# Optimization experiments

Measured on AMD Instinct MI355X. Metric: run time of the kernel, lower is better.

Reference implementation:

```python
import jax, jax.numpy as jnp
import numpy as np

N, E, G = 30000, 120000, 1000   # nodes, edges, graphs
IN, H, ED = 32, 64, 8           # in_dim, hidden, edge_dim


def setup_inputs() -> dict:
    key = jax.random.key(0)
    ks = iter(jax.random.split(key, 64))
    rn = lambda shp, s=0.05: jax.random.normal(next(ks), shp, dtype=jnp.float32) * s
    d = {}
    d["x"] = jax.random.normal(next(ks), (N, IN), dtype=jnp.float32)
    d["edge_index"] = jax.random.randint(next(ks), (2, E), 0, N)
    d["edge_attr"] = jax.random.normal(next(ks), (E, ED), dtype=jnp.float32)
    d["batch"] = jnp.sort(jax.random.randint(next(ks), (N,), 0, G))
    # layer 0: edge_nn maps edge_attr -> [H*IN], conv IN -> H
    d["ew1_0"] = rn((ED, H * IN)); d["eb1_0"] = jnp.zeros((H * IN,), jnp.float32)
    d["ew2_0"] = rn((H * IN, H * IN)); d["eb2_0"] = jnp.zeros((H * IN,), jnp.float32)
    d["root_0"] = rn((IN, H)); d["cb_0"] = jnp.zeros((H,), jnp.float32)
    # layers 1,2: edge_nn maps edge_attr -> [H*H], conv H -> H
    for i in (1, 2):
        d[f"ew1_{i}"] = rn((ED, H * H)); d[f"eb1_{i}"] = jnp.zeros((H * H,), jnp.float32)
        d[f"ew2_{i}"] = rn((H * H, H * H)); d[f"eb2_{i}"] = jnp.zeros((H * H,), jnp.float32)
        d[f"root_{i}"] = rn((H, H)); d[f"cb_{i}"] = jnp.zeros((H,), jnp.float32)
    # readout MLP
    d["mw1"] = rn((H, H)); d["mb1"] = jnp.zeros((H,), jnp.float32)
    d["mw2"] = rn((H, 1)); d["mb2"] = jnp.zeros((1,), jnp.float32)
    return d


def _nnconv(x, src, dst, edge_attr, ew1, eb1, ew2, eb2, root, cb, din, dout):
    # edge MLP -> per-edge weight matrix [E, din, dout]
    w = (jax.nn.relu(edge_attr @ ew1 + eb1) @ ew2 + eb2).reshape(-1, din, dout)
    # gather source features, per-edge matvec, scatter-mean to dest
    msg = jnp.einsum('ei,eio->eo', x[src], w)            # [E, dout]
    n = x.shape[0]
    s = jax.ops.segment_sum(msg, dst, num_segments=n)
    deg = jax.ops.segment_sum(jnp.ones((msg.shape[0],), msg.dtype), dst, num_segments=n)
    agg = s / jnp.maximum(deg, 1.0)[:, None]
    return agg + x @ root + cb


def reference(x, edge_index, edge_attr, batch,
              ew1_0, eb1_0, ew2_0, eb2_0, root_0, cb_0,
              ew1_1, eb1_1, ew2_1, eb2_1, root_1, cb_1,
              ew1_2, eb1_2, ew2_2, eb2_2, root_2, cb_2,
              mw1, mb1, mw2, mb2):
    src, dst = edge_index[0], edge_index[1]
    h = jax.nn.relu(_nnconv(x, src, dst, edge_attr, ew1_0, eb1_0, ew2_0, eb2_0, root_0, cb_0, IN, H))
    h = jax.nn.relu(_nnconv(h, src, dst, edge_attr, ew1_1, eb1_1, ew2_1, eb2_1, root_1, cb_1, H, H))
    h = jax.nn.relu(_nnconv(h, src, dst, edge_attr, ew1_2, eb1_2, ew2_2, eb2_2, root_2, cb_2, H, H))
    # global mean pool over graphs
    gs = jax.ops.segment_sum(h, batch, num_segments=G)
    cnt = jax.ops.segment_sum(jnp.ones((h.shape[0],), h.dtype), batch, num_segments=G)
    g = gs / jnp.maximum(cnt, 1.0)[:, None]
    # readout MLP (dropout inactive in eval)
    return jax.nn.relu(g @ mw1 + mb1) @ mw2 + mb2    # [G, 1]
```

## Files before the change

### kernel.cpp

```cpp
#include <hip/hip_runtime.h>
#include <cstdint>

#define N_TOT 30000
#define E_TOT 120000
#define G_TOT 1000

typedef unsigned short u16;
typedef unsigned int u32;
typedef __attribute__((ext_vector_type(8))) short short8;
typedef __attribute__((ext_vector_type(4))) float f32x4;

#define AS1 __attribute__((address_space(1)))
#define AS3 __attribute__((address_space(3)))

static __device__ __forceinline__ void gload_lds16(const void* g, void* l) {
  __builtin_amdgcn_global_load_lds((AS1 void*)(uintptr_t)g,
                                   (AS3 void*)(uint32_t)(uintptr_t)l, 16, 0, 0);
}

static __device__ __forceinline__ u16 f2bf(float f) {
  uint32_t u = __float_as_uint(f);
  uint32_t r = (u + 0x7fffu + ((u >> 16) & 1u)) >> 16;
  return (u16)r;
}
static __device__ __forceinline__ float bf2f(u16 v) {
  return __uint_as_float((uint32_t)v << 16);
}

__global__ void prep_kernel(const int* __restrict__ ei, const int* __restrict__ batch,
                            float* __restrict__ deg, float* __restrict__ gcnt,
                            int* __restrict__ sd) {
  int t = blockIdx.x * 256 + threadIdx.x;
  if (t < E_TOT) {
    atomicAdd(&deg[ei[E_TOT + t]], 1.0f);
    atomicAdd(&sd[ei[t]], 1);
  }
  if (t < N_TOT) atomicAdd(&gcnt[batch[t]], 1.0f);
}

__global__ void scan_kernel(const int* __restrict__ sd, int* __restrict__ off) {
  __shared__ int buf[1024];
  __shared__ int carry;
  const int t = threadIdx.x;
  if (t == 0) carry = 0;
  __syncthreads();
  for (int base = 0; base < N_TOT; base += 1024) {
    int v = base + t;
    int x = (v < N_TOT) ? sd[v] : 0;
    buf[t] = x;
    __syncthreads();
    for (int o = 1; o < 1024; o <<= 1) {
      int y = (t >= o) ? buf[t - o] : 0;
      __syncthreads();
      buf[t] += y;
      __syncthreads();
    }
    if (v < N_TOT) off[v] = carry + buf[t] - x;
    __syncthreads();
    if (t == 0) carry += buf[1023];
    __syncthreads();
  }
  if (t == 0) off[N_TOT] = carry;
}

__global__ void scatter_kernel(const int* __restrict__ ei, const float* __restrict__ ea,
                               const int* __restrict__ off, int* __restrict__ cur,
                               int* __restrict__ src_s, int* __restrict__ dst_s,
                               float* __restrict__ ea_s) {
  int e = blockIdx.x * 256 + threadIdx.x;
  if (e >= E_TOT) return;
  int s = ei[e];
  int pos = off[s] + atomicAdd(&cur[s], 1);
  src_s[pos] = s;
  dst_s[pos] = ei[E_TOT + e];
#pragma unroll
  for (int j = 0; j < 8; ++j) ea_s[(size_t)pos * 8 + j] = ea[(size_t)e * 8 + j];
}

__global__ void cvt_wp(const float* __restrict__ ew2, u16* __restrict__ wp,
                       int K, int DINp) {
  int idx = blockIdx.x * 256 + threadIdx.x;
  int c = idx & 127, kbh = idx >> 7;
  int kb = kbh >> 1, oh = kbh & 1;
  int k = kb * 4 + (c >> 5), o = oh * 32 + (c & 31);
  const float* src = ew2 + (size_t)k * (DINp * 64) + o;
  u16* dst = wp + (size_t)idx * DINp;
  for (int i = 0; i < DINp; ++i) dst[i] = f2bf(src[(size_t)i * 64]);
}

__global__ void cvt_w1(const float* __restrict__ ew1, float* __restrict__ ew1t, int K) {
  int i = blockIdx.x * 256 + threadIdx.x;
  if (i >= K * 8) return;
  int k = i >> 3, j = i & 7;
  ew1t[i] = ew1[(size_t)j * K + k];
}

template <int DIN>
__global__ __launch_bounds__(512, 4) void fused_conv(
    const u16* __restrict__ Wp, const float* __restrict__ ew1t,
    const float* __restrict__ eb1, const float* __restrict__ eb2,
    const float* __restrict__ xin, const float* __restrict__ eas,
    const int* __restrict__ src_s, const int* __restrict__ dst_s,
    const int* __restrict__ node_off, float* __restrict__ agg, int K) {
  constexpr int KF = DIN / 32;
  constexpr int NB = DIN / 8;
  constexpr int L_XB = 0;
  constexpr int L_WP = 64 * DIN * 2;
  constexpr int L_MS = L_WP + 128 * DIN * 2;
  constexpr int L_HS = L_MS + 16384;
  constexpr int L_VL = L_HS + 4096;
  __shared__ char smem[L_VL + 2048];

  const int t = threadIdx.x;
  const int lane = t & 63, wave = t >> 6;
  const int u = lane & 15, q = lane >> 4;
  const int grp = blockIdx.x >> 1, oh = blockIdx.x & 1;
  const int v0 = grp * 64;
  const int e0 = node_off[v0];
  const int v1 = (v0 + 64 < N_TOT) ? v0 + 64 : N_TOT;
  int Eblk = node_off[v1] - e0;
  if (Eblk > 512) Eblk = 512;

  {
    int row = t >> 3, i0 = (t & 7) * (DIN / 8);
    u16* xb = (u16*)(smem + L_XB) + row * DIN + i0;
    int vg = v0 + row;
#pragma unroll
    for (int j = 0; j < DIN / 8; ++j)
      xb[j] = (vg < N_TOT) ? f2bf(xin[(size_t)vg * DIN + i0 + j]) : (u16)0;
  }
  f32x4 ea0 = (f32x4){0.f, 0.f, 0.f, 0.f}, ea1 = (f32x4){0.f, 0.f, 0.f, 0.f};
  {
    int vl = 0;
    if (t < Eblk) {
      const f32x4* s = (const f32x4*)(eas + (size_t)(e0 + t) * 8);
      ea0 = s[0];
      ea1 = s[1];
      vl = src_s[e0 + t] - v0;
    }
    ((int*)(smem + L_VL))[t] = vl;
  }
  __syncthreads();

  short8 bfr[4][KF];
#pragma unroll
  for (int vt = 0; vt < 4; ++vt)
#pragma unroll
    for (int kf = 0; kf < KF; ++kf)
      bfr[vt][kf] =
          *(const short8*)(smem + L_XB + ((vt * 16 + u) * DIN + (kf * 4 + q) * 8) * 2);

  const int oq = t & 1;
  int vofs[2], vswz[2], slotp[2];
#pragma unroll
  for (int p = 0; p < 2; ++p) {
    int s = (t >> 1) + p * 256;
    slotp[p] = s;
    int vl = ((int*)(smem + L_VL))[s];
    vofs[p] = L_MS + vl * 256;
    vswz[p] = vl & 7;
  }
  f32x4 msg[2][4];
#pragma unroll
  for (int p = 0; p < 2; ++p)
#pragma unroll
    for (int j = 0; j < 4; ++j) msg[p][j] = (f32x4){0.f, 0.f, 0.f, 0.f};

  const size_t slab = (size_t)128 * DIN;
  const int nsteps = K >> 2;
  for (int kb = 0; kb < nsteps; ++kb) {
    const u16* gsl = Wp + (size_t)(kb * 2 + oh) * slab;
#pragma unroll
    for (int j = 0; j < NB / 4; ++j) {
      int s = j * 512 + t;
      int c = s / NB, ib = s % NB;
      gload_lds16(gsl + (c * NB + (ib ^ (c & (NB - 1)))) * 8, smem + L_WP + s * 16);
    }
    {
      const int kk = kb * 4;
      ushort4 hv;
      u16* hp = (u16*)&hv;
#pragma unroll
      for (int kc = 0; kc < 4; ++kc) {
        int k = kk + kc;
        const float* wr = ew1t + (size_t)k * 8;
        float a = eb1[k];
        a += ea0.x * wr[0] + ea0.y * wr[1] + ea0.z * wr[2] + ea0.w * wr[3];
        a += ea1.x * wr[4] + ea1.y * wr[5] + ea1.z * wr[6] + ea1.w * wr[7];
        hp[kc] = f2bf(a > 0.f ? a : 0.f);
      }
      *(ushort4*)(smem + L_HS + t * 8) = hv;
    }
    __syncthreads();

    {
      f32x4 acc[4];
#pragma unroll
      for (int vt = 0; vt < 4; ++vt) acc[vt] = (f32x4){0.f, 0.f, 0.f, 0.f};
      const int crow = wave * 16 + u;
#pragma unroll
      for (int kf = 0; kf < KF; ++kf) {
        short8 afr = *(const short8*)(
            smem + L_WP + (crow * DIN + (((kf * 4 + q) ^ (crow & (NB - 1))) * 8)) * 2);
#pragma unroll
        for (int vt = 0; vt < 4; ++vt)
          acc[vt] = __builtin_amdgcn_mfma_f32_16x16x32_bf16(afr, bfr[vt][kf], acc[vt], 0, 0, 0);
      }
#pragma unroll
      for (int vt = 0; vt < 4; ++vt) {
        int v = vt * 16 + u;
        uint2 pk;
        pk.x = ((u32)f2bf(acc[vt].y) << 16) | f2bf(acc[vt].x);
        pk.y = ((u32)f2bf(acc[vt].w) << 16) | f2bf(acc[vt].z);
        int bbG = ((wave << 1) | (q >> 1)) ^ (v & 7);
        *(uint2*)(smem + L_MS + v * 256 + bbG * 16 + (q & 1) * 8) = pk;
      }
    }
    __syncthreads();

#pragma unroll
    for (int p = 0; p < 2; ++p) {
      if (wave * 32 + p * 256 < Eblk) {
        ushort4 h4 = *(const ushort4*)(smem + L_HS + slotp[p] * 8);
        const u16* hp = (const u16*)&h4;
#pragma unroll
        for (int kc = 0; kc < 4; ++kc) {
          float h = bf2f(hp[kc]);
#pragma unroll
          for (int s = 0; s < 2; ++s) {
            int bb = (kc * 4 + oq * 2 + s) ^ vswz[p];
            uint4 m8 = *(const uint4*)(smem + vofs[p] + bb * 16);
            f32x4 lo, hi;
            lo.x = __uint_as_float(m8.x << 16);
            lo.y = __uint_as_float(m8.x & 0xffff0000u);
            lo.z = __uint_as_float(m8.y << 16);
            lo.w = __uint_as_float(m8.y & 0xffff0000u);
            hi.x = __uint_as_float(m8.z << 16);
            hi.y = __uint_as_float(m8.z & 0xffff0000u);
            hi.z = __uint_as_float(m8.w << 16);
            hi.w = __uint_as_float(m8.w & 0xffff0000u);
            msg[p][s * 2 + 0] += h * lo;
            msg[p][s * 2 + 1] += h * hi;
          }
        }
      }
    }
    __syncthreads();
  }

  {
    int v = t >> 3, o4 = (t & 7) * 4;
    f32x4 acc = (f32x4){0.f, 0.f, 0.f, 0.f};
    const u16* xb = (const u16*)(smem + L_XB) + v * DIN;
    const float* ep = eb2 + oh * 32 + o4;
    for (int i = 0; i < DIN; ++i) {
      float xv = bf2f(xb[i]);
      f32x4 w4 = *(const f32x4*)(ep + (size_t)i * 64);
      acc += xv * w4;
    }
    *(f32x4*)(smem + L_MS + (v * 32 + o4) * 4) = acc;
  }
  __syncthreads();

#pragma unroll
  for (int p = 0; p < 2; ++p) {
    int slot = slotp[p];
    if (slot < Eblk) {
      int d = dst_s[e0 + slot];
      int vl = (vofs[p] - L_MS) >> 8;
      float* ap = agg + (size_t)d * 64 + oh * 32 + oq * 16;
      const float* bt = (const float*)(smem + L_MS) + vl * 32 + oq * 16;
#pragma unroll
      for (int j = 0; j < 4; ++j) {
        f32x4 m = msg[p][j];
        atomicAdd(ap + j * 4 + 0, m.x + bt[j * 4 + 0]);
        atomicAdd(ap + j * 4 + 1, m.y + bt[j * 4 + 1]);
        atomicAdd(ap + j * 4 + 2, m.z + bt[j * 4 + 2]);
        atomicAdd(ap + j * 4 + 3, m.w + bt[j * 4 + 3]);
      }
    }
  }
}

__global__ void node_update(const float* __restrict__ agg, const float* __restrict__ deg,
                            const float* __restrict__ xin, const float* __restrict__ root,
                            const float* __restrict__ cbv, float* __restrict__ xout,
                            int din) {
  __shared__ float rl[4096];
  const int t = threadIdx.x;
  for (int i = t; i < din * 64; i += 256) rl[i] = root[i];
  __syncthreads();
  const int o = t & 63;
  const int n = blockIdx.x * 4 + (t >> 6);
  if (n >= N_TOT) return;
  float acc = cbv[o];
  for (int i = 0; i < din; ++i) acc += xin[(size_t)n * din + i] * rl[i * 64 + o];
  float d = deg[n];
  d = d > 1.f ? d : 1.f;
  acc += agg[(size_t)n * 64 + o] / d;
  xout[(size_t)n * 64 + o] = acc > 0.f ? acc : 0.f;
}

__global__ void pool_kernel(const float* __restrict__ x3, const int* __restrict__ batch,
                            float* __restrict__ gsum) {
  int t = blockIdx.x * 256 + threadIdx.x;
  if (t >= N_TOT * 64) return;
  int n = t >> 6, o = t & 63;
  atomicAdd(&gsum[(size_t)batch[n] * 64 + o], x3[t]);
}

__global__ void readout_kernel(const float* __restrict__ gsum, const float* __restrict__ gcnt,
                               const float* __restrict__ mw1, const float* __restrict__ mb1,
                               const float* __restrict__ mw2, const float* __restrict__ mb2,
                               float* __restrict__ out) {
  __shared__ float gv[4][64];
  const int t = threadIdx.x;
  const int o = t & 63, loc = t >> 6;
  const int g = blockIdx.x * 4 + loc;
  float v = 0.f;
  if (g < G_TOT) {
    float c = gcnt[g];
    c = c > 1.f ? c : 1.f;
    v = gsum[(size_t)g * 64 + o] / c;
  }
  gv[loc][o] = v;
  __syncthreads();
  float acc = mb1[o];
  for (int i = 0; i < 64; ++i) acc += gv[loc][i] * mw1[i * 64 + o];
  acc = acc > 0.f ? acc : 0.f;
  float p = acc * mw2[o];
#pragma unroll
  for (int off = 32; off > 0; off >>= 1) p += __shfl_down(p, off, 64);
  if (o == 0 && g < G_TOT) out[g] = p + mb2[0];
}

extern "C" void kernel_launch(void* const* d_in, const int* in_sizes, int n_in,
                              void* d_out, int out_size, void* d_ws, size_t ws_size,
                              hipStream_t stream) {
  const float* x     = (const float*)d_in[0];
  const int*   ei    = (const int*)d_in[1];
  const float* ea    = (const float*)d_in[2];
  const int*   batch = (const int*)d_in[3];
  const float* ew1[3] = {(const float*)d_in[4],  (const float*)d_in[10], (const float*)d_in[16]};
  const float* eb1[3] = {(const float*)d_in[5],  (const float*)d_in[11], (const float*)d_in[17]};
  const float* ew2[3] = {(const float*)d_in[6],  (const float*)d_in[12], (const float*)d_in[18]};
  const float* eb2[3] = {(const float*)d_in[7],  (const float*)d_in[13], (const float*)d_in[19]};
  const float* root[3] = {(const float*)d_in[8],  (const float*)d_in[14], (const float*)d_in[20]};
  const float* cbv[3]  = {(const float*)d_in[9],  (const float*)d_in[15], (const float*)d_in[21]};
  const float* mw1 = (const float*)d_in[22];
  const float* mb1 = (const float*)d_in[23];
  const float* mw2 = (const float*)d_in[24];
  const float* mb2 = (const float*)d_in[25];
  float* out = (float*)d_out;

  char* p = (char*)d_ws;
  auto carve = [&p](size_t bytes) {
    char* r = p;
    p += (bytes + 255) & ~(size_t)255;
    return r;
  };
  u16*   wp   = (u16*)carve((size_t)4096 * 64 * 64 * 2);
  float* ew1t = (float*)carve((size_t)4096 * 8 * 4);
  float* x1   = (float*)carve((size_t)N_TOT * 64 * 4);
  float* x2   = (float*)carve((size_t)N_TOT * 64 * 4);
  float* x3   = (float*)carve((size_t)N_TOT * 64 * 4);
  float* agg  = (float*)carve((size_t)N_TOT * 64 * 4);
  float* deg  = (float*)carve((size_t)N_TOT * 4);
  float* gsum = (float*)carve((size_t)G_TOT * 64 * 4);
  float* gcnt = (float*)carve((size_t)G_TOT * 4);
  int*   sd   = (int*)carve((size_t)N_TOT * 4);
  int*   noff = (int*)carve((size_t)(N_TOT + 1) * 4);
  int*   cur  = (int*)carve((size_t)N_TOT * 4);
  int*   srcs = (int*)carve((size_t)E_TOT * 4);
  int*   dsts = (int*)carve((size_t)E_TOT * 4);
  float* eass = (float*)carve((size_t)E_TOT * 8 * 4);

  hipMemsetAsync(deg, 0, (size_t)N_TOT * 4, stream);
  hipMemsetAsync(gsum, 0, (size_t)G_TOT * 64 * 4, stream);
  hipMemsetAsync(gcnt, 0, (size_t)G_TOT * 4, stream);
  hipMemsetAsync(sd, 0, (size_t)N_TOT * 4, stream);
  hipMemsetAsync(cur, 0, (size_t)N_TOT * 4, stream);

  prep_kernel<<<(E_TOT + 255) / 256, 256, 0, stream>>>(ei, batch, deg, gcnt, sd);
  scan_kernel<<<1, 1024, 0, stream>>>(sd, noff);
  scatter_kernel<<<(E_TOT + 255) / 256, 256, 0, stream>>>(ei, ea, noff, cur, srcs, dsts, eass);

  const float* xin_l[3]  = {x, x1, x2};
  float*       xout_l[3] = {x1, x2, x3};
  const int Ks[3]   = {2048, 4096, 4096};
  const int dins[3] = {32, 64, 64};
  const int grid_fused = ((N_TOT + 63) / 64) * 2;

  for (int L = 0; L < 3; ++L) {
    const int K = Ks[L], din = dins[L];
    cvt_wp<<<(K * 64) / 256, 256, 0, stream>>>(ew2[L], wp, K, din);
    cvt_w1<<<(K * 8 + 255) / 256, 256, 0, stream>>>(ew1[L], ew1t, K);
    hipMemsetAsync(agg, 0, (size_t)N_TOT * 64 * 4, stream);
    if (din == 32)
      fused_conv<32><<<grid_fused, 512, 0, stream>>>(wp, ew1t, eb1[L], eb2[L], xin_l[L],
                                                     eass, srcs, dsts, noff, agg, K);
    else
      fused_conv<64><<<grid_fused, 512, 0, stream>>>(wp, ew1t, eb1[L], eb2[L], xin_l[L],
                                                     eass, srcs, dsts, noff, agg, K);
    node_update<<<(N_TOT + 3) / 4, 256, 0, stream>>>(agg, deg, xin_l[L], root[L], cbv[L],
                                                     xout_l[L], din);
  }
  pool_kernel<<<(N_TOT * 64 + 255) / 256, 256, 0, stream>>>(x3, batch, gsum);
  readout_kernel<<<(G_TOT + 3) / 4, 256, 0, stream>>>(gsum, gcnt, mw1, mb1, mw2, mb2, out);
}
```

Baseline: 11.88 ms.

## Store intermediate messages as fp16 with k-interleaved padded layout for packed FMA

Reorders the precomputed weight slab so the four k values of each output sit next to each other. The per-node MFMA results and hidden activations are now stored in LDS as fp16 pairs in padded rows (272 bytes) instead of bf16 in XOR-swizzled rows. Each edge thread then reads contiguous 16-byte chunks and does dot-products over k with unpacked half2 values, dropping the swizzle arithmetic and the bf16 shift/mask unpacking. The intermediates now use fp16 rounding in place of bf16, which gives more mantissa bits but less range, and the padding is there to limit LDS bank conflicts.

```diff
diff --git a/kernel.cpp b/kernel.cpp
--- a/kernel.cpp
+++ b/kernel.cpp
@@ -1,4 +1,5 @@
 #include <hip/hip_runtime.h>
+#include <hip/hip_fp16.h>
 #include <cstdint>
 
 #define N_TOT 30000
@@ -25,6 +26,14 @@
 }
 static __device__ __forceinline__ float bf2f(u16 v) {
   return __uint_as_float((uint32_t)v << 16);
+}
+
+static __device__ __forceinline__ u32 packh2(float a, float b) {
+  __half2 h = __floats2half2_rn(a, b);
+  return __builtin_bit_cast(u32, h);
+}
+static __device__ __forceinline__ float2 unph2(u32 v) {
+  return __half22float2(__builtin_bit_cast(__half2, v));
 }
 
 __global__ void prep_kernel(const int* __restrict__ ei, const int* __restrict__ batch,
@@ -82,7 +91,7 @@
   int idx = blockIdx.x * 256 + threadIdx.x;
   int c = idx & 127, kbh = idx >> 7;
   int kb = kbh >> 1, oh = kbh & 1;
-  int k = kb * 4 + (c >> 5), o = oh * 32 + (c & 31);
+  int k = kb * 4 + (c & 3), o = oh * 32 + (c >> 2);
   const float* src = ew2 + (size_t)k * (DINp * 64) + o;
   u16* dst = wp + (size_t)idx * DINp;
   for (int i = 0; i < DINp; ++i) dst[i] = f2bf(src[(size_t)i * 64]);
@@ -104,10 +113,11 @@
     const int* __restrict__ node_off, float* __restrict__ agg, int K) {
   constexpr int KF = DIN / 32;
   constexpr int NB = DIN / 8;
+  constexpr int MROW = 272;
   constexpr int L_XB = 0;
   constexpr int L_WP = 64 * DIN * 2;
   constexpr int L_MS = L_WP + 128 * DIN * 2;
-  constexpr int L_HS = L_MS + 16384;
+  constexpr int L_HS = L_MS + 64 * MROW;
   constexpr int L_VL = L_HS + 4096;
   __shared__ char smem[L_VL + 2048];
 
@@ -151,20 +161,21 @@
           *(const short8*)(smem + L_XB + ((vt * 16 + u) * DIN + (kf * 4 + q) * 8) * 2);
 
   const int oq = t & 1;
-  int vofs[2], vswz[2], slotp[2];
+  int mbase[2], hbase[2], vls[2], slotp[2];
 #pragma unroll
   for (int p = 0; p < 2; ++p) {
     int s = (t >> 1) + p * 256;
     slotp[p] = s;
     int vl = ((int*)(smem + L_VL))[s];
-    vofs[p] = L_MS + vl * 256;
-    vswz[p] = vl & 7;
-  }
-  f32x4 msg[2][4];
+    vls[p] = vl;
+    mbase[p] = L_MS + vl * MROW + oq * 136;
+    hbase[p] = L_HS + s * 8;
+  }
+  float acc[2][16];
 #pragma unroll
   for (int p = 0; p < 2; ++p)
 #pragma unroll
-    for (int j = 0; j < 4; ++j) msg[p][j] = (f32x4){0.f, 0.f, 0.f, 0.f};
+    for (int j = 0; j < 16; ++j) acc[p][j] = 0.f;
 
   const size_t slab = (size_t)128 * DIN;
   const int nsteps = K >> 2;
@@ -178,8 +189,7 @@
     }
     {
       const int kk = kb * 4;
-      ushort4 hv;
-      u16* hp = (u16*)&hv;
+      float hv[4];
 #pragma unroll
       for (int kc = 0; kc < 4; ++kc) {
         int k = kk + kc;
@@ -187,16 +197,19 @@
         float a = eb1[k];
         a += ea0.x * wr[0] + ea0.y * wr[1] + ea0.z * wr[2] + ea0.w * wr[3];
         a += ea1.x * wr[4] + ea1.y * wr[5] + ea1.z * wr[6] + ea1.w * wr[7];
-        hp[kc] = f2bf(a > 0.f ? a : 0.f);
+        hv[kc] = a > 0.f ? a : 0.f;
       }
-      *(ushort4*)(smem + L_HS + t * 8) = hv;
+      uint2 hw;
+      hw.x = packh2(hv[0], hv[1]);
+      hw.y = packh2(hv[2], hv[3]);
+      *(uint2*)(smem + L_HS + t * 8) = hw;
     }
     __syncthreads();
 
     {
-      f32x4 acc[4];
-#pragma unroll
-      for (int vt = 0; vt < 4; ++vt) acc[vt] = (f32x4){0.f, 0.f, 0.f, 0.f};
+      f32x4 acm[4];
+#pragma unroll
+      for (int vt = 0; vt < 4; ++vt) acm[vt] = (f32x4){0.f, 0.f, 0.f, 0.f};
       const int crow = wave * 16 + u;
 #pragma unroll
       for (int kf = 0; kf < KF; ++kf) {
@@ -204,16 +217,17 @@
             smem + L_WP + (crow * DIN + (((kf * 4 + q) ^ (crow & (NB - 1))) * 8)) * 2);
 #pragma unroll
         for (int vt = 0; vt < 4; ++vt)
-          acc[vt] = __builtin_amdgcn_mfma_f32_16x16x32_bf16(afr, bfr[vt][kf], acc[vt], 0, 0, 0);
+          acm[vt] = __builtin_amdgcn_mfma_f32_16x16x32_bf16(afr, bfr[vt][kf], acm[vt], 0, 0, 0);
       }
+      const int opr = wave * 4 + q;
+      const int off = opr * 8 + (opr >> 4) * 8;
 #pragma unroll
       for (int vt = 0; vt < 4; ++vt) {
         int v = vt * 16 + u;
         uint2 pk;
-        pk.x = ((u32)f2bf(acc[vt].y) << 16) | f2bf(acc[vt].x);
-        pk.y = ((u32)f2bf(acc[vt].w) << 16) | f2bf(acc[vt].z);
-        int bbG = ((wave << 1) | (q >> 1)) ^ (v & 7);
-        *(uint2*)(smem + L_MS + v * 256 + bbG * 16 + (q & 1) * 8) = pk;
+        pk.x = packh2(acm[vt].x, acm[vt].y);
+        pk.y = packh2(acm[vt].z, acm[vt].w);
+        *(uint2*)(smem + L_MS + v * MROW + off) = pk;
       }
     }
     __syncthreads();
@@ -221,27 +235,28 @@
 #pragma unroll
     for (int p = 0; p < 2; ++p) {
       if (wave * 32 + p * 256 < Eblk) {
-        ushort4 h4 = *(const ushort4*)(smem + L_HS + slotp[p] * 8);
-        const u16* hp = (const u16*)&h4;
-#pragma unroll
-        for (int kc = 0; kc < 4; ++kc) {
-          float h = bf2f(hp[kc]);
-#pragma unroll
-          for (int s = 0; s < 2; ++s) {
-            int bb = (kc * 4 + oq * 2 + s) ^ vswz[p];
-            uint4 m8 = *(const uint4*)(smem + vofs[p] + bb * 16);
-            f32x4 lo, hi;
-            lo.x = __uint_as_float(m8.x << 16);
-            lo.y = __uint_as_float(m8.x & 0xffff0000u);
-            lo.z = __uint_as_float(m8.y << 16);
-            lo.w = __uint_as_float(m8.y & 0xffff0000u);
-            hi.x = __uint_as_float(m8.z << 16);
-            hi.y = __uint_as_float(m8.z & 0xffff0000u);
-            hi.z = __uint_as_float(m8.w << 16);
-            hi.w = __uint_as_float(m8.w & 0xffff0000u);
-            msg[p][s * 2 + 0] += h * lo;
-            msg[p][s * 2 + 1] += h * hi;
-          }
+        uint2 hu = *(const uint2*)(smem + hbase[p]);
+        float2 h01 = unph2(hu.x);
+        float2 h23 = unph2(hu.y);
+        const char* mr = smem + mbase[p];
+#pragma unroll
+        for (int m = 0; m < 8; ++m) {
+          uint4 m8 = *(const uint4*)(mr + m * 16);
+          float2 a0 = unph2(m8.x);
+          float2 a1 = unph2(m8.y);
+          float2 b0 = unph2(m8.z);
+          float2 b1 = unph2(m8.w);
+          float s0 = acc[p][2 * m], s1 = acc[p][2 * m + 1];
+          s0 += a0.x * h01.x;
+          s0 += a0.y * h01.y;
+          s0 += a1.x * h23.x;
+          s0 += a1.y * h23.y;
+          s1 += b0.x * h01.x;
+          s1 += b0.y * h01.y;
+          s1 += b1.x * h23.x;
+          s1 += b1.y * h23.y;
+          acc[p][2 * m] = s0;
+          acc[p][2 * m + 1] = s1;
         }
       }
     }
@@ -250,15 +265,15 @@
 
   {
     int v = t >> 3, o4 = (t & 7) * 4;
-    f32x4 acc = (f32x4){0.f, 0.f, 0.f, 0.f};
+    f32x4 acb = (f32x4){0.f, 0.f, 0.f, 0.f};
     const u16* xb = (const u16*)(smem + L_XB) + v * DIN;
     const float* ep = eb2 + oh * 32 + o4;
     for (int i = 0; i < DIN; ++i) {
       float xv = bf2f(xb[i]);
       f32x4 w4 = *(const f32x4*)(ep + (size_t)i * 64);
-      acc += xv * w4;
-    }
-    *(f32x4*)(smem + L_MS + (v * 32 + o4) * 4) = acc;
+      acb += xv * w4;
+    }
+    *(f32x4*)(smem + L_MS + (v * 32 + o4) * 4) = acb;
   }
   __syncthreads();
 
@@ -267,17 +282,10 @@
     int slot = slotp[p];
     if (slot < Eblk) {
       int d = dst_s[e0 + slot];
-      int vl = (vofs[p] - L_MS) >> 8;
       float* ap = agg + (size_t)d * 64 + oh * 32 + oq * 16;
-      const float* bt = (const float*)(smem + L_MS) + vl * 32 + oq * 16;
-#pragma unroll
-      for (int j = 0; j < 4; ++j) {
-        f32x4 m = msg[p][j];
-        atomicAdd(ap + j * 4 + 0, m.x + bt[j * 4 + 0]);
-        atomicAdd(ap + j * 4 + 1, m.y + bt[j * 4 + 1]);
-        atomicAdd(ap + j * 4 + 2, m.z + bt[j * 4 + 2]);
-        atomicAdd(ap + j * 4 + 3, m.w + bt[j * 4 + 3]);
-      }
+      const float* bt = (const float*)(smem + L_MS) + vls[p] * 32 + oq * 16;
+#pragma unroll
+      for (int j = 0; j < 16; ++j) atomicAdd(ap + j, acc[p][j] + bt[j]);
     }
   }
 }
```

Measured after the change: 24.52 ms. 2.06x slower.
